# Kernel optimization log

Hardware: AMD Instinct MI355X
Metric: run time of the kernel (lower is better)

Reference implementation:

```python
import jax, jax.numpy as jnp
import numpy as np

B, S, H, D = 4, 2048, 8, 64


def init_offset(size, a=0.02, b=0.1, lo=8.0, hi=14.0):
    if size == 1:
        return jnp.array([(hi - lo) / 2], dtype=jnp.float32)
    x = jnp.log(jnp.expm1(jnp.linspace(a, b, size)))
    x = (x - x.min()) / (x.max() - x.min())
    return (x * abs(hi - lo) + lo).astype(jnp.float32)


def setup_inputs() -> dict:
    key = jax.random.key(0)
    k1, k2, k3 = jax.random.split(key, 3)
    qk = jax.random.normal(k1, (B, S, 2, H, D), dtype=jnp.float32)
    v = jax.random.normal(k2, (B, S, H, D), dtype=jnp.float32)
    n = jax.random.normal(k3, (B, S, H), dtype=jnp.float32)
    offset = init_offset(H)  # learned per-head offset parameter
    return {"qk": qk, "v": v, "n": n, "offset": offset}


def reference(qk, v, n, offset):
    # approx_fn = elu(x) + 1 (feature map), norm_fn = softplus, scale_B=True
    q = jax.nn.elu(qk[:, :, 0]) + 1.0  # (B,S,H,D)
    k = jax.nn.elu(qk[:, :, 1]) + 1.0  # (B,S,H,D)
    scale = 1.0 / jnp.sqrt(jnp.asarray(q.shape[-1], q.dtype))
    # outer product per position then causal prefix-sum over sequence
    kv = jnp.einsum('bshd,bsht->bshdt', k * scale, v)  # (B,S,H,D,D)
    kv = jnp.cumsum(kv, axis=1)
    out = jnp.einsum('bshd,bshdt->bsht', q, kv)  # (B,S,H,D)
    norm = jnp.exp(-jax.nn.softplus(n + offset))  # (B,S,H)
    return norm[:, :, :, None] * out
```

## Files before the change

kernel.cpp:

```cpp
#include <hip/hip_runtime.h>
#include <cstdint>

#define BB 4
#define SS 2048
#define HH 8
#define DD 64
#define CC 64
#define NCK (SS/CC)
#define BHH (BB*HH)

typedef __attribute__((ext_vector_type(8))) short  short8;
typedef __attribute__((ext_vector_type(4))) float  f32x4;
typedef __attribute__((ext_vector_type(4))) unsigned short us4;

__device__ __forceinline__ float elu1(float x) {
    return x > 0.f ? x + 1.f : __expf(x);
}
__device__ __forceinline__ unsigned short f2bf(float f) {
    unsigned int u = __float_as_uint(f);
    u += 0x7FFFu + ((u >> 16) & 1u);
    return (unsigned short)(u >> 16);
}
__device__ __forceinline__ float bf2f(unsigned short h) {
    return __uint_as_float(((unsigned int)h) << 16);
}
#define SWZ(r,c) ((r) * DD + ((c) ^ (((r) & 7) << 3)))

template<int M0, int M1>
__device__ __forceinline__ void xpose4(float v[4], int lane) {
    {
        const bool hi = (lane & M0) != 0;
        float x0 = hi ? v[0] : v[1];
        float x1 = hi ? v[2] : v[3];
        float r0 = __shfl_xor(x0, M0);
        float r1 = __shfl_xor(x1, M0);
        if (hi) { v[0] = r0; v[2] = r1; } else { v[1] = r0; v[3] = r1; }
    }
    {
        const bool hi = (lane & M1) != 0;
        float x0 = hi ? v[0] : v[2];
        float x1 = hi ? v[1] : v[3];
        float r0 = __shfl_xor(x0, M1);
        float r1 = __shfl_xor(x1, M1);
        if (hi) { v[0] = r0; v[1] = r1; } else { v[2] = r0; v[3] = r1; }
    }
}

__device__ __forceinline__ unsigned long long pack4bf(const float v[4]) {
    unsigned long long r;
    r  = (unsigned long long)f2bf(v[0]);
    r |= (unsigned long long)f2bf(v[1]) << 16;
    r |= (unsigned long long)f2bf(v[2]) << 32;
    r |= (unsigned long long)f2bf(v[3]) << 48;
    return r;
}

__global__ __launch_bounds__(256) void kv_chunk_kernel(
    const float* __restrict__ qk, const float* __restrict__ v,
    unsigned short* __restrict__ qws, unsigned short* __restrict__ kws,
    unsigned short* __restrict__ vtws, unsigned short* __restrict__ Sws)
{
    const int blk = blockIdx.x;
    const int bh = blk / NCK, c = blk % NCK;
    const int b = bh / HH, h = bh % HH;
    const int s0 = c * CC;

    __shared__ __align__(16) unsigned short kT[CC * DD];
    __shared__ __align__(16) unsigned short vT[CC * DD];

    const int tid = threadIdx.x, lane = tid & 63;

#pragma unroll
    for (int iter = 0; iter < 4; ++iter) {
        const int it = iter * 256 + tid;
        const int r = it >> 4, c0 = (it & 15) * 4;
        const int g = lane >> 4;
        const int rb = r - g;

        const size_t qrow = (((size_t)(b * SS + s0 + r) * 2 + 0) * HH + h) * DD;

        float4 fq = *reinterpret_cast<const float4*>(qk + qrow + c0);
        us4 uq; uq.x = f2bf(elu1(fq.x)); uq.y = f2bf(elu1(fq.y));
                uq.z = f2bf(elu1(fq.z)); uq.w = f2bf(elu1(fq.w));
        *reinterpret_cast<us4*>(qws + (size_t)blk * 4096 + SWZ(r, c0)) = uq;

        float4 fk = *reinterpret_cast<const float4*>(qk + qrow + (size_t)HH * DD + c0);
        float kv4[4] = { elu1(fk.x) * 0.125f, elu1(fk.y) * 0.125f,
                         elu1(fk.z) * 0.125f, elu1(fk.w) * 0.125f };
        us4 uk; uk.x = f2bf(kv4[0]); uk.y = f2bf(kv4[1]);
                uk.z = f2bf(kv4[2]); uk.w = f2bf(kv4[3]);
        *reinterpret_cast<us4*>(kws + (size_t)blk * 4096 + SWZ(r, c0)) = uk;
        xpose4<16, 32>(kv4, lane);
        *reinterpret_cast<unsigned long long*>(&kT[SWZ(c0 + g, rb)]) = pack4bf(kv4);

        float4 fv = *reinterpret_cast<const float4*>(
            v + ((size_t)(b * SS + s0 + r) * HH + h) * DD + c0);
        float vv4[4] = { fv.x, fv.y, fv.z, fv.w };
        xpose4<16, 32>(vv4, lane);
        *reinterpret_cast<unsigned long long*>(&vT[SWZ(c0 + g, rb)]) = pack4bf(vv4);
    }
    __syncthreads();

#pragma unroll
    for (int j = 0; j < 2; ++j) {
        const int slot = j * 256 + tid;
        *reinterpret_cast<short8*>(vtws + (size_t)blk * 4096 + slot * 8) =
            *reinterpret_cast<const short8*>(&vT[slot * 8]);
    }

    const int lr = lane & 15, lk = (lane >> 4) * 8;
    const int wid = tid >> 6, mbase = wid * 16;
    f32x4 sc[4] = {};
#pragma unroll
    for (int kk = 0; kk < 2; ++kk) {
        short8 a = *reinterpret_cast<const short8*>(&vT[SWZ(mbase + lr, kk * 32 + lk)]);
#pragma unroll
        for (int nb = 0; nb < 4; ++nb) {
            short8 bk = *reinterpret_cast<const short8*>(&kT[SWZ(nb * 16 + lr, kk * 32 + lk)]);
            sc[nb] = __builtin_amdgcn_mfma_f32_16x16x32_bf16(a, bk, sc[nb], 0, 0, 0);
        }
    }
    const int crow = (lane >> 4) * 4;
#pragma unroll
    for (int nb = 0; nb < 4; ++nb) {
        float cv[4] = { sc[nb][0], sc[nb][1], sc[nb][2], sc[nb][3] };
        xpose4<1, 2>(cv, lane);
        const int t  = mbase + crow + (lane & 3);
        const int d0 = nb * 16 + (lr & ~3);
        *reinterpret_cast<unsigned long long*>(
            Sws + (size_t)blk * 4096 + SWZ(t, d0)) = pack4bf(cv);
    }
}

__global__ __launch_bounds__(256) void prefix_kernel(unsigned short* __restrict__ Sws)
{
    const int bh = blockIdx.x >> 2, part = blockIdx.x & 3;
    const int e = part * 1024 + threadIdx.x * 4;
    unsigned short* p = Sws + (size_t)bh * NCK * 4096 + e;

    float r0 = 0.f, r1 = 0.f, r2 = 0.f, r3 = 0.f;
#pragma unroll
    for (int c = 0; c < NCK; ++c) {
        us4 a = *reinterpret_cast<const us4*>(p + (size_t)c * 4096);
        us4 o; o.x = f2bf(r0); o.y = f2bf(r1); o.z = f2bf(r2); o.w = f2bf(r3);
        *reinterpret_cast<us4*>(p + (size_t)c * 4096) = o;
        r0 += bf2f(a.x); r1 += bf2f(a.y); r2 += bf2f(a.z); r3 += bf2f(a.w);
    }
}

__global__ __launch_bounds__(256) void out_kernel(
    const unsigned short* __restrict__ qws, const unsigned short* __restrict__ kws,
    const unsigned short* __restrict__ vtws, const unsigned short* __restrict__ Sws,
    const float* __restrict__ nrm, const float* __restrict__ offset,
    float* __restrict__ out)
{
    const int blk = blockIdx.x;
    const int bh = blk / NCK, c = blk % NCK;
    const int b = bh / HH, h = bh % HH;
    const int s0 = c * CC;

    __shared__ __align__(16) unsigned short qb[CC * DD];
    __shared__ __align__(16) unsigned short kb[CC * DD];
    __shared__ __align__(16) unsigned short vT[CC * DD];
    __shared__ __align__(16) unsigned short st[CC * DD];

    const int tid = threadIdx.x, lane = tid & 63;
    const int wid = tid >> 6;

    {
        const unsigned short* gsrc[4] = {
            qws + (size_t)blk * 4096, kws + (size_t)blk * 4096,
            vtws + (size_t)blk * 4096, Sws + (size_t)blk * 4096 };
        unsigned short* ldst[4] = { qb, kb, vT, st };
#pragma unroll
        for (int bu = 0; bu < 4; ++bu) {
#pragma unroll
            for (int j = 0; j < 2; ++j) {
                const unsigned short* gp = gsrc[bu] + (size_t)(j * 256 + tid) * 8;
                __builtin_amdgcn_global_load_lds(
                    (const __attribute__((address_space(1))) void*)gp,
                    (__attribute__((address_space(3))) void*)(ldst[bu] + j * 2048 + wid * 512),
                    16, 0, 0);
            }
        }
    }

    const int lr    = lane & 15;
    const int lk    = (lane >> 4) * 8;
    const int mbase = wid * 16;
    const int crow  = (lane >> 4) * 4;

    const float off = offset[h];
    float nv[4];
#pragma unroll
    for (int r = 0; r < 4; ++r) {
        const int s = s0 + mbase + crow + r;
        nv[r] = nrm[(size_t)(b * SS + s) * HH + h] + off;
    }
#pragma unroll
    for (int r = 0; r < 4; ++r) nv[r] = 1.f / (1.f + __expf(nv[r]));

    __syncthreads();

    f32x4 acc[4] = {};
    f32x4 as4[4] = {};
#pragma unroll
    for (int kk = 0; kk < 2; ++kk) {
        short8 aq = *reinterpret_cast<const short8*>(&qb[SWZ(mbase + lr, kk * 32 + lk)]);
#pragma unroll
        for (int nb = 0; nb < 4; ++nb) {
            short8 bs = *reinterpret_cast<const short8*>(&st[SWZ(nb * 16 + lr, kk * 32 + lk)]);
            acc[nb] = __builtin_amdgcn_mfma_f32_16x16x32_bf16(aq, bs, acc[nb], 0, 0, 0);
            short8 bk = *reinterpret_cast<const short8*>(&kb[SWZ(nb * 16 + lr, kk * 32 + lk)]);
            as4[nb] = __builtin_amdgcn_mfma_f32_16x16x32_bf16(aq, bk, as4[nb], 0, 0, 0);
        }
    }
    __syncthreads();

#pragma unroll
    for (int nb = 0; nb < 4; ++nb) {
#pragma unroll
        for (int r = 0; r < 4; ++r) {
            const int s_loc = mbase + crow + r;
            const int s2    = nb * 16 + lr;
            const float val = (s2 <= s_loc) ? as4[nb][r] : 0.f;
            kb[SWZ(s_loc, s2)] = f2bf(val);
        }
    }

#pragma unroll
    for (int kk = 0; kk < 2; ++kk) {
        short8 aa = *reinterpret_cast<const short8*>(&kb[SWZ(mbase + lr, kk * 32 + lk)]);
#pragma unroll
        for (int nb = 0; nb < 4; ++nb) {
            short8 bv = *reinterpret_cast<const short8*>(&vT[SWZ(nb * 16 + lr, kk * 32 + lk)]);
            acc[nb] = __builtin_amdgcn_mfma_f32_16x16x32_bf16(aa, bv, acc[nb], 0, 0, 0);
        }
    }

#pragma unroll
    for (int nb = 0; nb < 4; ++nb) {
#pragma unroll
        for (int r = 0; r < 4; ++r) {
            const int s = s0 + mbase + crow + r;
            out[((size_t)(b * SS + s) * HH + h) * DD + nb * 16 + lr] = acc[nb][r] * nv[r];
        }
    }
}

extern "C" void kernel_launch(void* const* d_in, const int* in_sizes, int n_in,
                              void* d_out, int out_size, void* d_ws, size_t ws_size,
                              hipStream_t stream) {
    const float* qk     = (const float*)d_in[0];
    const float* v      = (const float*)d_in[1];
    const float* nrm    = (const float*)d_in[2];
    const float* offset = (const float*)d_in[3];
    float* out = (float*)d_out;

    const size_t TILE = (size_t)BHH * NCK * 4096;
    unsigned short* qws  = (unsigned short*)d_ws;
    unsigned short* kws  = qws  + TILE;
    unsigned short* vtws = kws  + TILE;
    unsigned short* Sws  = vtws + TILE;

    kv_chunk_kernel<<<dim3(BHH * NCK), dim3(256), 0, stream>>>(qk, v, qws, kws, vtws, Sws);
    prefix_kernel<<<dim3(BHH * 4), dim3(256), 0, stream>>>(Sws);
    out_kernel<<<dim3(BHH * NCK), dim3(256), 0, stream>>>(qws, kws, vtws, Sws, nrm, offset, out);
}
```

Measured before the change: 112.7 us.

## Fold chunk-state prefix sum into output kernel and load q directly

Removes the separate prefix-scan kernel. Each output block now sums all earlier chunk states itself, reading them from workspace and accumulating in fp32 registers. q is no longer staged through a bf16 workspace: the output kernel reads it from the input and applies elu+1 in place. This saves one launch and the q write/read round trip. In exchange, the redundant prefix reads grow quadratically with chunk index (up to 31 chunk states per block), and launch bounds now ask for 4 blocks per SM.

```diff
diff --git a/kernel.cpp b/kernel.cpp
--- a/kernel.cpp
+++ b/kernel.cpp
@@ -12,6 +12,7 @@
 typedef __attribute__((ext_vector_type(8))) short  short8;
 typedef __attribute__((ext_vector_type(4))) float  f32x4;
 typedef __attribute__((ext_vector_type(4))) unsigned short us4;
+typedef unsigned long long u64;
 
 __device__ __forceinline__ float elu1(float x) {
     return x > 0.f ? x + 1.f : __expf(x);
@@ -46,19 +47,19 @@
     }
 }
 
-__device__ __forceinline__ unsigned long long pack4bf(const float v[4]) {
-    unsigned long long r;
-    r  = (unsigned long long)f2bf(v[0]);
-    r |= (unsigned long long)f2bf(v[1]) << 16;
-    r |= (unsigned long long)f2bf(v[2]) << 32;
-    r |= (unsigned long long)f2bf(v[3]) << 48;
+__device__ __forceinline__ u64 pack4bf(const float v[4]) {
+    u64 r;
+    r  = (u64)f2bf(v[0]);
+    r |= (u64)f2bf(v[1]) << 16;
+    r |= (u64)f2bf(v[2]) << 32;
+    r |= (u64)f2bf(v[3]) << 48;
     return r;
 }
 
-__global__ __launch_bounds__(256) void kv_chunk_kernel(
+__global__ __launch_bounds__(256) void state_kernel(
     const float* __restrict__ qk, const float* __restrict__ v,
-    unsigned short* __restrict__ qws, unsigned short* __restrict__ kws,
-    unsigned short* __restrict__ vtws, unsigned short* __restrict__ Sws)
+    unsigned short* __restrict__ kws, unsigned short* __restrict__ vtws,
+    u64* __restrict__ Sws)
 {
     const int blk = blockIdx.x;
     const int bh = blk / NCK, c = blk % NCK;
@@ -77,27 +78,22 @@
         const int g = lane >> 4;
         const int rb = r - g;
 
-        const size_t qrow = (((size_t)(b * SS + s0 + r) * 2 + 0) * HH + h) * DD;
-
-        float4 fq = *reinterpret_cast<const float4*>(qk + qrow + c0);
-        us4 uq; uq.x = f2bf(elu1(fq.x)); uq.y = f2bf(elu1(fq.y));
-                uq.z = f2bf(elu1(fq.z)); uq.w = f2bf(elu1(fq.w));
-        *reinterpret_cast<us4*>(qws + (size_t)blk * 4096 + SWZ(r, c0)) = uq;
-
-        float4 fk = *reinterpret_cast<const float4*>(qk + qrow + (size_t)HH * DD + c0);
+        const size_t krow = (((size_t)(b * SS + s0 + r) * 2 + 1) * HH + h) * DD;
+
+        float4 fk = *reinterpret_cast<const float4*>(qk + krow + c0);
         float kv4[4] = { elu1(fk.x) * 0.125f, elu1(fk.y) * 0.125f,
                          elu1(fk.z) * 0.125f, elu1(fk.w) * 0.125f };
         us4 uk; uk.x = f2bf(kv4[0]); uk.y = f2bf(kv4[1]);
                 uk.z = f2bf(kv4[2]); uk.w = f2bf(kv4[3]);
         *reinterpret_cast<us4*>(kws + (size_t)blk * 4096 + SWZ(r, c0)) = uk;
         xpose4<16, 32>(kv4, lane);
-        *reinterpret_cast<unsigned long long*>(&kT[SWZ(c0 + g, rb)]) = pack4bf(kv4);
+        *reinterpret_cast<u64*>(&kT[SWZ(c0 + g, rb)]) = pack4bf(kv4);
 
         float4 fv = *reinterpret_cast<const float4*>(
             v + ((size_t)(b * SS + s0 + r) * HH + h) * DD + c0);
         float vv4[4] = { fv.x, fv.y, fv.z, fv.w };
         xpose4<16, 32>(vv4, lane);
-        *reinterpret_cast<unsigned long long*>(&vT[SWZ(c0 + g, rb)]) = pack4bf(vv4);
+        *reinterpret_cast<u64*>(&vT[SWZ(c0 + g, rb)]) = pack4bf(vv4);
     }
     __syncthreads();
 
@@ -127,32 +123,15 @@
         xpose4<1, 2>(cv, lane);
         const int t  = mbase + crow + (lane & 3);
         const int d0 = nb * 16 + (lr & ~3);
-        *reinterpret_cast<unsigned long long*>(
-            Sws + (size_t)blk * 4096 + SWZ(t, d0)) = pack4bf(cv);
-    }
-}
-
-__global__ __launch_bounds__(256) void prefix_kernel(unsigned short* __restrict__ Sws)
-{
-    const int bh = blockIdx.x >> 2, part = blockIdx.x & 3;
-    const int e = part * 1024 + threadIdx.x * 4;
-    unsigned short* p = Sws + (size_t)bh * NCK * 4096 + e;
-
-    float r0 = 0.f, r1 = 0.f, r2 = 0.f, r3 = 0.f;
-#pragma unroll
-    for (int c = 0; c < NCK; ++c) {
-        us4 a = *reinterpret_cast<const us4*>(p + (size_t)c * 4096);
-        us4 o; o.x = f2bf(r0); o.y = f2bf(r1); o.z = f2bf(r2); o.w = f2bf(r3);
-        *reinterpret_cast<us4*>(p + (size_t)c * 4096) = o;
-        r0 += bf2f(a.x); r1 += bf2f(a.y); r2 += bf2f(a.z); r3 += bf2f(a.w);
-    }
-}
-
-__global__ __launch_bounds__(256) void out_kernel(
-    const unsigned short* __restrict__ qws, const unsigned short* __restrict__ kws,
-    const unsigned short* __restrict__ vtws, const unsigned short* __restrict__ Sws,
-    const float* __restrict__ nrm, const float* __restrict__ offset,
-    float* __restrict__ out)
+        Sws[(size_t)blk * 1024 + (SWZ(t, d0) >> 2)] = pack4bf(cv);
+    }
+}
+
+__global__ __launch_bounds__(256, 4) void out_kernel(
+    const float* __restrict__ qk, const float* __restrict__ nrm,
+    const float* __restrict__ offset,
+    const unsigned short* __restrict__ kws, const unsigned short* __restrict__ vtws,
+    const u64* __restrict__ Sws, float* __restrict__ out)
 {
     const int blk = blockIdx.x;
     const int bh = blk / NCK, c = blk % NCK;
@@ -162,18 +141,17 @@
     __shared__ __align__(16) unsigned short qb[CC * DD];
     __shared__ __align__(16) unsigned short kb[CC * DD];
     __shared__ __align__(16) unsigned short vT[CC * DD];
-    __shared__ __align__(16) unsigned short st[CC * DD];
+    __shared__ __align__(16) unsigned short stk[CC * DD];
 
     const int tid = threadIdx.x, lane = tid & 63;
     const int wid = tid >> 6;
 
     {
-        const unsigned short* gsrc[4] = {
-            qws + (size_t)blk * 4096, kws + (size_t)blk * 4096,
-            vtws + (size_t)blk * 4096, Sws + (size_t)blk * 4096 };
-        unsigned short* ldst[4] = { qb, kb, vT, st };
-#pragma unroll
-        for (int bu = 0; bu < 4; ++bu) {
+        const unsigned short* gsrc[2] = { kws + (size_t)blk * 4096,
+                                          vtws + (size_t)blk * 4096 };
+        unsigned short* ldst[2] = { kb, vT };
+#pragma unroll
+        for (int bu = 0; bu < 2; ++bu) {
 #pragma unroll
             for (int j = 0; j < 2; ++j) {
                 const unsigned short* gp = gsrc[bu] + (size_t)(j * 256 + tid) * 8;
@@ -185,6 +163,17 @@
         }
     }
 
+#pragma unroll
+    for (int iter = 0; iter < 4; ++iter) {
+        const int it = iter * 256 + tid;
+        const int r = it >> 4, c0 = (it & 15) * 4;
+        const size_t qrow = (((size_t)(b * SS + s0 + r) * 2 + 0) * HH + h) * DD;
+        float4 fq = *reinterpret_cast<const float4*>(qk + qrow + c0);
+        us4 uq; uq.x = f2bf(elu1(fq.x)); uq.y = f2bf(elu1(fq.y));
+                uq.z = f2bf(elu1(fq.z)); uq.w = f2bf(elu1(fq.w));
+        *reinterpret_cast<us4*>(&qb[SWZ(r, c0)]) = uq;
+    }
+
     const int lr    = lane & 15;
     const int lk    = (lane >> 4) * 8;
     const int mbase = wid * 16;
@@ -197,8 +186,44 @@
         const int s = s0 + mbase + crow + r;
         nv[r] = nrm[(size_t)(b * SS + s) * HH + h] + off;
     }
-#pragma unroll
-    for (int r = 0; r < 4; ++r) nv[r] = 1.f / (1.f + __expf(nv[r]));
+
+    float run[16] = {};
+    {
+        const u64* base = Sws + (size_t)bh * NCK * 1024 + (size_t)tid * 4;
+        int j = 0;
+        for (; j + 2 <= c; j += 2) {
+            const u64* s0p = base + (size_t)j * 1024;
+            const u64* s1p = s0p + 1024;
+            u64 x0[4], x1[4];
+#pragma unroll
+            for (int w2 = 0; w2 < 4; ++w2) { x0[w2] = s0p[w2]; x1[w2] = s1p[w2]; }
+#pragma unroll
+            for (int w2 = 0; w2 < 4; ++w2) {
+                run[w2 * 4 + 0] += bf2f((unsigned short)(x0[w2]))       + bf2f((unsigned short)(x1[w2]));
+                run[w2 * 4 + 1] += bf2f((unsigned short)(x0[w2] >> 16)) + bf2f((unsigned short)(x1[w2] >> 16));
+                run[w2 * 4 + 2] += bf2f((unsigned short)(x0[w2] >> 32)) + bf2f((unsigned short)(x1[w2] >> 32));
+                run[w2 * 4 + 3] += bf2f((unsigned short)(x0[w2] >> 48)) + bf2f((unsigned short)(x1[w2] >> 48));
+            }
+        }
+        if (j < c) {
+            const u64* s0p = base + (size_t)j * 1024;
+#pragma unroll
+            for (int w2 = 0; w2 < 4; ++w2) {
+                u64 x = s0p[w2];
+                run[w2 * 4 + 0] += bf2f((unsigned short)(x));
+                run[w2 * 4 + 1] += bf2f((unsigned short)(x >> 16));
+                run[w2 * 4 + 2] += bf2f((unsigned short)(x >> 32));
+                run[w2 * 4 + 3] += bf2f((unsigned short)(x >> 48));
+            }
+        }
+    }
+    u64* stk64 = reinterpret_cast<u64*>(stk);
+#pragma unroll
+    for (int w2 = 0; w2 < 4; ++w2) {
+        float cv[4] = { run[w2 * 4 + 0], run[w2 * 4 + 1],
+                        run[w2 * 4 + 2], run[w2 * 4 + 3] };
+        stk64[(size_t)tid * 4 + w2] = pack4bf(cv);
+    }
 
     __syncthreads();
 
@@ -209,7 +234,7 @@
         short8 aq = *reinterpret_cast<const short8*>(&qb[SWZ(mbase + lr, kk * 32 + lk)]);
 #pragma unroll
         for (int nb = 0; nb < 4; ++nb) {
-            short8 bs = *reinterpret_cast<const short8*>(&st[SWZ(nb * 16 + lr, kk * 32 + lk)]);
+            short8 bs = *reinterpret_cast<const short8*>(&stk[SWZ(nb * 16 + lr, kk * 32 + lk)]);
             acc[nb] = __builtin_amdgcn_mfma_f32_16x16x32_bf16(aq, bs, acc[nb], 0, 0, 0);
             short8 bk = *reinterpret_cast<const short8*>(&kb[SWZ(nb * 16 + lr, kk * 32 + lk)]);
             as4[nb] = __builtin_amdgcn_mfma_f32_16x16x32_bf16(aq, bk, as4[nb], 0, 0, 0);
@@ -238,6 +263,8 @@
         }
     }
 
+#pragma unroll
+    for (int r = 0; r < 4; ++r) nv[r] = 1.f / (1.f + __expf(nv[r]));
 #pragma unroll
     for (int nb = 0; nb < 4; ++nb) {
 #pragma unroll
@@ -258,12 +285,10 @@
     float* out = (float*)d_out;
 
     const size_t TILE = (size_t)BHH * NCK * 4096;
-    unsigned short* qws  = (unsigned short*)d_ws;
-    unsigned short* kws  = qws  + TILE;
-    unsigned short* vtws = kws  + TILE;
-    unsigned short* Sws  = vtws + TILE;
-
-    kv_chunk_kernel<<<dim3(BHH * NCK), dim3(256), 0, stream>>>(qk, v, qws, kws, vtws, Sws);
-    prefix_kernel<<<dim3(BHH * 4), dim3(256), 0, stream>>>(Sws);
-    out_kernel<<<dim3(BHH * NCK), dim3(256), 0, stream>>>(qws, kws, vtws, Sws, nrm, offset, out);
-}
+    unsigned short* kws  = (unsigned short*)d_ws;
+    unsigned short* vtws = kws + TILE;
+    u64* Sws = (u64*)(vtws + TILE);
+
+    state_kernel<<<dim3(BHH * NCK), dim3(256), 0, stream>>>(qk, v, kws, vtws, Sws);
+    out_kernel<<<dim3(BHH * NCK), dim3(256), 0, stream>>>(qk, nrm, offset, kws, vtws, Sws, out);
+}
```

Result: slower. 118.2 us (+4.9%).
